# Kernel optimization log

Hardware: AMD Instinct MI355X
Metric: run time of the kernel (lower is better)

The kernel has to match this reference:

```python
import jax, jax.numpy as jnp
import numpy as np

B, J = 1000000, 17

def setup_inputs() -> dict:
    key = jax.random.key(0)
    k1, k2, k3 = jax.random.split(key, 3)
    output = jax.random.uniform(k1, (B, J, 3), dtype=jnp.float32)  # class channel in (0,1) for BCE
    reg_gt = jax.random.uniform(k2, (B, J, 2), dtype=jnp.float32)
    class_gt = (jax.random.uniform(k3, (B, J)) > 0.5).astype(jnp.float32)  # binary {0,1}
    target = jnp.concatenate([reg_gt, class_gt[:, :, None]], axis=2)
    return {"output": output, "target": target}

def reference(output, target):
    reg_pred = output[:, :, :2]          # [B,J,2]
    class_pred = output[:, :, 2]         # [B,J]
    reg_gt = target[:, :, :2]
    class_gt = target[:, :, 2]

    # nn.BCELoss (mean reduction), with torch's log clamp at -100
    log_p = jnp.maximum(jnp.log(class_pred), -100.0)
    log_1mp = jnp.maximum(jnp.log1p(-class_pred), -100.0)
    loss_class = -jnp.mean(class_gt * log_p + (1.0 - class_gt) * log_1mp)

    # masked_fill(mask < 0.5, 0) on BOTH pred and gt -> masked entries contribute 0 to MSE sum
    keep = class_pred[:, :, None] >= 0.5                       # [B,J,1] broadcast over 2 coords
    diff = jnp.where(keep, reg_pred - reg_gt, 0.0)             # [B,J,2]
    sq_sum = jnp.sum(diff * diff, axis=(1, 2))                 # [B]

    # per-batch joint count: 1 + #(class_gt == 1)
    num_joints = 1.0 + jnp.sum((class_gt == 1.0).astype(diff.dtype), axis=1)  # [B]

    loss_reg = jnp.mean(0.5 * sq_sum / num_joints)  # == (sum over batch)/batch_size
    return loss_class + loss_reg
```

## Files before the change

### kernel.cpp

```cpp
#include <hip/hip_runtime.h>
#include <hip/hip_bf16.h>
#include <stdint.h>

#define J_JOINTS 17
#define ROW_F 51
#define BLOCK 256
#define TILE_ROWS 32
#define TILE_F (TILE_ROWS * ROW_F)
#define TILE_CHUNKS (TILE_F / 4)
#define GRID 1536

__device__ __forceinline__ void gld_lds16(const float* g, float* l) {
    __builtin_amdgcn_global_load_lds(
        (const __attribute__((address_space(1))) void*)g,
        (__attribute__((address_space(3))) void*)l,
        16, 0, 0);
}

__global__ __launch_bounds__(BLOCK) void loss_main_kernel(
    const float* __restrict__ outp,
    const float* __restrict__ tgt,
    double* __restrict__ acc,
    int B)
{
    __shared__ float so[2][TILE_F];
    __shared__ float st[2][TILE_F];

    const int tid = threadIdx.x;
    const int r8  = tid >> 3;
    const int q   = tid & 7;

    float cls_acc = 0.0f;
    float reg_acc = 0.0f;

    const int tiles_total = (B + TILE_ROWS - 1) / TILE_ROWS;

    auto stage_async = [&](int row0, int buf) {
        const float* go = outp + row0 * ROW_F;
        const float* gt = tgt  + row0 * ROW_F;
        float* lo = so[buf];
        float* lt = st[buf];
        #pragma unroll
        for (int j = 0; j < 2; ++j) {
            const int i = tid + j * BLOCK;
            if (i < TILE_CHUNKS) {
                gld_lds16(go + i * 4, lo + i * 4);
                gld_lds16(gt + i * 4, lt + i * 4);
            }
        }
    };
    auto stage_sync = [&](int row0, int rows_valid, int buf) {
        const float* go = outp + row0 * ROW_F;
        const float* gt = tgt  + row0 * ROW_F;
        const int nv = rows_valid * ROW_F;
        const int n4 = nv >> 2;
        for (int i = tid; i < n4; i += BLOCK) {
            reinterpret_cast<float4*>(so[buf])[i] = reinterpret_cast<const float4*>(go)[i];
            reinterpret_cast<float4*>(st[buf])[i] = reinterpret_cast<const float4*>(gt)[i];
        }
        const int tb = n4 << 2;
        if (tid < nv - tb) {
            so[buf][tb + tid] = go[tb + tid];
            st[buf][tb + tid] = gt[tb + tid];
        }
    };
    auto stage = [&](int tk, int buf) {
        const int row0 = tk * TILE_ROWS;
        if (row0 + TILE_ROWS <= B) stage_async(row0, buf);
        else                       stage_sync(row0, B - row0, buf);
    };

    int tk  = blockIdx.x;
    int cur = 0;

    if (tk < tiles_total) stage(tk, 0);
    asm volatile("s_waitcnt vmcnt(0)" ::: "memory");
    __syncthreads();

    while (tk < tiles_total) {
        const int tn = tk + GRID;
        if (tn < tiles_total) stage(tn, cur ^ 1);

        const int rows_valid = min(TILE_ROWS, B - tk * TILE_ROWS);
        float sq = 0.0f;
        float nj = 0.0f;
        if (r8 < rows_valid) {
            const float* lo = so[cur] + r8 * ROW_F + q * 6;
            const float* lt = st[cur] + r8 * ROW_F + q * 6;
            #pragma unroll
            for (int k = 0; k < 2; ++k) {
                const float ox = lo[3*k + 0];
                const float oy = lo[3*k + 1];
                const float oz = lo[3*k + 2];
                const float tx = lt[3*k + 0];
                const float ty = lt[3*k + 1];
                const float tz = lt[3*k + 2];

                const bool gt1 = (tz == 1.0f);
                cls_acc += fmaxf(__logf(gt1 ? oz : (1.0f - oz)), -100.0f);

                const bool keep = (oz >= 0.5f);
                const float d0 = keep ? (ox - tx) : 0.0f;
                const float d1 = keep ? (oy - ty) : 0.0f;
                sq = fmaf(d0, d0, fmaf(d1, d1, sq));
                nj += gt1 ? 1.0f : 0.0f;
            }
            if (q == 7) {
                const float ox = lo[6 + 0];
                const float oy = lo[6 + 1];
                const float oz = lo[6 + 2];
                const float tx = lt[6 + 0];
                const float ty = lt[6 + 1];
                const float tz = lt[6 + 2];

                const bool gt1 = (tz == 1.0f);
                cls_acc += fmaxf(__logf(gt1 ? oz : (1.0f - oz)), -100.0f);

                const bool keep = (oz >= 0.5f);
                const float d0 = keep ? (ox - tx) : 0.0f;
                const float d1 = keep ? (oy - ty) : 0.0f;
                sq = fmaf(d0, d0, fmaf(d1, d1, sq));
                nj += gt1 ? 1.0f : 0.0f;
            }
        }
        sq += __shfl_xor(sq, 1, 64);  nj += __shfl_xor(nj, 1, 64);
        sq += __shfl_xor(sq, 2, 64);  nj += __shfl_xor(nj, 2, 64);
        sq += __shfl_xor(sq, 4, 64);  nj += __shfl_xor(nj, 4, 64);
        if (q == 0 && r8 < rows_valid) {
            reg_acc += __fdividef(0.5f * sq, 1.0f + nj);
        }

        asm volatile("s_waitcnt vmcnt(0)" ::: "memory");
        __syncthreads();
        cur ^= 1;
        tk = tn;
    }

    #pragma unroll
    for (int m = 1; m < 64; m <<= 1) {
        cls_acc += __shfl_xor(cls_acc, m, 64);
        reg_acc += __shfl_xor(reg_acc, m, 64);
    }
    __shared__ float s_cls[BLOCK / 64];
    __shared__ float s_reg[BLOCK / 64];
    const int wid = tid >> 6;
    if ((tid & 63) == 0) {
        s_cls[wid] = cls_acc;
        s_reg[wid] = reg_acc;
    }
    __syncthreads();
    if (tid == 0) {
        float c = 0.0f, r = 0.0f;
        #pragma unroll
        for (int w = 0; w < BLOCK / 64; ++w) { c += s_cls[w]; r += s_reg[w]; }
        atomicAdd(&acc[0], (double)c);
        atomicAdd(&acc[1], (double)r);
    }
}

__global__ void loss_finalize_kernel(const double* __restrict__ acc,
                                     float* __restrict__ out, int B)
{
    const double cls_sum = acc[0];
    const double reg_sum = acc[1];
    const double loss_class = -cls_sum / ((double)B * (double)J_JOINTS);
    const double loss_reg   = reg_sum / (double)B;
    out[0] = (float)(loss_class + loss_reg);
}

extern "C" void kernel_launch(void* const* d_in, const int* in_sizes, int n_in,
                              void* d_out, int out_size, void* d_ws, size_t ws_size,
                              hipStream_t stream) {
    const float* outp = (const float*)d_in[0];
    const float* tgt  = (const float*)d_in[1];
    float* out = (float*)d_out;
    const int B = in_sizes[0] / (J_JOINTS * 3);

    double* acc = (double*)d_ws;
    hipMemsetAsync(acc, 0, 2 * sizeof(double), stream);

    loss_main_kernel<<<GRID, BLOCK, 0, stream>>>(outp, tgt, acc, B);
    loss_finalize_kernel<<<1, 1, 0, stream>>>(acc, out, B);
}
```

Before: 101.6 us.

## Deepen async LDS pipeline to four buffers with per-wave counted waits

```diff
diff --git a/kernel.cpp b/kernel.cpp
--- a/kernel.cpp
+++ b/kernel.cpp
@@ -8,7 +8,9 @@
 #define TILE_ROWS 32
 #define TILE_F (TILE_ROWS * ROW_F)
 #define TILE_CHUNKS (TILE_F / 4)
-#define GRID 1536
+#define NBUF 4
+#define CHUNKS_PER_WAVE 102
+#define GRID 768
 
 __device__ __forceinline__ void gld_lds16(const float* g, float* l) {
     __builtin_amdgcn_global_load_lds(
@@ -23,70 +25,58 @@
     double* __restrict__ acc,
     int B)
 {
-    __shared__ float so[2][TILE_F];
-    __shared__ float st[2][TILE_F];
+    __shared__ float so[NBUF][TILE_F];
+    __shared__ float st[NBUF][TILE_F];
 
     const int tid = threadIdx.x;
+    const int wv  = tid >> 6;
+    const int ln  = tid & 63;
     const int r8  = tid >> 3;
     const int q   = tid & 7;
 
     float cls_acc = 0.0f;
     float reg_acc = 0.0f;
 
-    const int tiles_total = (B + TILE_ROWS - 1) / TILE_ROWS;
+    const int tiles_full = B / TILE_ROWS;
+    const int nt = (tiles_full > (int)blockIdx.x)
+                 ? (tiles_full - (int)blockIdx.x + GRID - 1) / GRID : 0;
 
-    auto stage_async = [&](int row0, int buf) {
-        const float* go = outp + row0 * ROW_F;
-        const float* gt = tgt  + row0 * ROW_F;
-        float* lo = so[buf];
-        float* lt = st[buf];
-        #pragma unroll
-        for (int j = 0; j < 2; ++j) {
-            const int i = tid + j * BLOCK;
-            if (i < TILE_CHUNKS) {
-                gld_lds16(go + i * 4, lo + i * 4);
-                gld_lds16(gt + i * 4, lt + i * 4);
-            }
+    auto stage = [&](int i) {
+        const int tile = (int)blockIdx.x + i * GRID;
+        const int buf  = i & (NBUF - 1);
+        const float* go = outp + tile * TILE_F;
+        const float* gt = tgt  + tile * TILE_F;
+        const int c0 = wv * CHUNKS_PER_WAVE + ln;
+        gld_lds16(go + c0 * 4, &so[buf][c0 * 4]);
+        gld_lds16(gt + c0 * 4, &st[buf][c0 * 4]);
+        const int c1 = c0 + 64;
+        if (ln < CHUNKS_PER_WAVE - 64) {
+            gld_lds16(go + c1 * 4, &so[buf][c1 * 4]);
+            gld_lds16(gt + c1 * 4, &st[buf][c1 * 4]);
         }
     };
-    auto stage_sync = [&](int row0, int rows_valid, int buf) {
-        const float* go = outp + row0 * ROW_F;
-        const float* gt = tgt  + row0 * ROW_F;
-        const int nv = rows_valid * ROW_F;
-        const int n4 = nv >> 2;
-        for (int i = tid; i < n4; i += BLOCK) {
-            reinterpret_cast<float4*>(so[buf])[i] = reinterpret_cast<const float4*>(go)[i];
-            reinterpret_cast<float4*>(st[buf])[i] = reinterpret_cast<const float4*>(gt)[i];
-        }
-        const int tb = n4 << 2;
-        if (tid < nv - tb) {
-            so[buf][tb + tid] = go[tb + tid];
-            st[buf][tb + tid] = gt[tb + tid];
-        }
-    };
-    auto stage = [&](int tk, int buf) {
-        const int row0 = tk * TILE_ROWS;
-        if (row0 + TILE_ROWS <= B) stage_async(row0, buf);
-        else                       stage_sync(row0, B - row0, buf);
-    };
 
-    int tk  = blockIdx.x;
-    int cur = 0;
+    if (nt > 0) stage(0);
+    if (nt > 1) stage(1);
+    if (nt > 2) stage(2);
 
-    if (tk < tiles_total) stage(tk, 0);
-    asm volatile("s_waitcnt vmcnt(0)" ::: "memory");
-    __syncthreads();
+    for (int i = 0; i < nt; ++i) {
+        if (i + 3 < nt) stage(i + 3);
 
-    while (tk < tiles_total) {
-        const int tn = tk + GRID;
-        if (tn < tiles_total) stage(tn, cur ^ 1);
+        const int newer = min(nt - 1 - i, 3);
+        if      (newer == 3) asm volatile("s_waitcnt vmcnt(12)" ::: "memory");
+        else if (newer == 2) asm volatile("s_waitcnt vmcnt(8)"  ::: "memory");
+        else if (newer == 1) asm volatile("s_waitcnt vmcnt(4)"  ::: "memory");
+        else                 asm volatile("s_waitcnt vmcnt(0)"  ::: "memory");
+        __builtin_amdgcn_s_barrier();
+        __builtin_amdgcn_sched_barrier(0);
 
-        const int rows_valid = min(TILE_ROWS, B - tk * TILE_ROWS);
+        const int buf = i & (NBUF - 1);
         float sq = 0.0f;
         float nj = 0.0f;
-        if (r8 < rows_valid) {
-            const float* lo = so[cur] + r8 * ROW_F + q * 6;
-            const float* lt = st[cur] + r8 * ROW_F + q * 6;
+        {
+            const float* lo = &so[buf][r8 * ROW_F + q * 6];
+            const float* lt = &st[buf][r8 * ROW_F + q * 6];
             #pragma unroll
             for (int k = 0; k < 2; ++k) {
                 const float ox = lo[3*k + 0];
@@ -126,14 +116,35 @@
         sq += __shfl_xor(sq, 1, 64);  nj += __shfl_xor(nj, 1, 64);
         sq += __shfl_xor(sq, 2, 64);  nj += __shfl_xor(nj, 2, 64);
         sq += __shfl_xor(sq, 4, 64);  nj += __shfl_xor(nj, 4, 64);
-        if (q == 0 && r8 < rows_valid) {
+        if (q == 0) {
             reg_acc += __fdividef(0.5f * sq, 1.0f + nj);
         }
 
-        asm volatile("s_waitcnt vmcnt(0)" ::: "memory");
-        __syncthreads();
-        cur ^= 1;
-        tk = tn;
+        __builtin_amdgcn_sched_barrier(0);
+        __builtin_amdgcn_s_barrier();
+    }
+
+    const int tail0 = tiles_full * TILE_ROWS;
+    if (blockIdx.x == 0 && tid < (B - tail0)) {
+        const int b = tail0 + tid;
+        float sq = 0.f, nj = 0.f;
+        for (int j = 0; j < J_JOINTS; ++j) {
+            const int base = b * ROW_F + 3*j;
+            const float ox = outp[base + 0];
+            const float oy = outp[base + 1];
+            const float oz = outp[base + 2];
+            const float tx = tgt[base + 0];
+            const float ty = tgt[base + 1];
+            const float tz = tgt[base + 2];
+            const bool gt1 = (tz == 1.0f);
+            cls_acc += fmaxf(__logf(gt1 ? oz : (1.0f - oz)), -100.0f);
+            const bool keep = (oz >= 0.5f);
+            const float d0 = keep ? (ox - tx) : 0.0f;
+            const float d1 = keep ? (oy - ty) : 0.0f;
+            sq = fmaf(d0, d0, fmaf(d1, d1, sq));
+            nj += gt1 ? 1.0f : 0.0f;
+        }
+        reg_acc += __fdividef(0.5f * sq, 1.0f + nj);
     }
 
     #pragma unroll
@@ -143,10 +154,9 @@
     }
     __shared__ float s_cls[BLOCK / 64];
     __shared__ float s_reg[BLOCK / 64];
-    const int wid = tid >> 6;
-    if ((tid & 63) == 0) {
-        s_cls[wid] = cls_acc;
-        s_reg[wid] = reg_acc;
+    if (ln == 0) {
+        s_cls[wv] = cls_acc;
+        s_reg[wv] = reg_acc;
     }
     __syncthreads();
     if (tid == 0) {
```

New measurement: 92.71 us. -8.7%, faster.
